# Optimization experiments

Measured on AMD Instinct MI355X. Metric: run time of the kernel, lower is better.

The kernel has to match this reference:

```python
import jax, jax.numpy as jnp
import numpy as np

INPUT_DIM = 1024
OUTPUT_DIM = 1024
DEGREE = 8


def setup_inputs() -> dict:
    key = jax.random.key(0)
    k1, k2 = jax.random.split(key)
    x = jax.random.normal(k1, (8192, INPUT_DIM), dtype=jnp.float32)
    std = 1.0 / (INPUT_DIM * (DEGREE + 1))
    cheby_coeffs = jax.random.normal(k2, (INPUT_DIM, OUTPUT_DIM, DEGREE + 1), dtype=jnp.float32) * std
    return {"x": x, "cheby_coeffs": cheby_coeffs}


def reference(x, cheby_coeffs):
    # x: [B, I]; cheby_coeffs: [I, O, D+1]
    degree = cheby_coeffs.shape[-1] - 1
    t = jnp.clip(jnp.tanh(x), -0.999, 0.999)            # [B, I]
    theta = jnp.arccos(t)[..., None]                     # [B, I, 1]
    arange = jnp.arange(degree + 1, dtype=x.dtype)       # [D+1]
    basis = jnp.cos(theta * arange)                      # [B, I, D+1] Chebyshev T_d(t)
    y = jnp.einsum('bid,iod->bo', basis, cheby_coeffs)   # [B, O]
    return y
```

## Files before the change

kernel.cpp:

```cpp
#include <hip/hip_runtime.h>
#include <stdint.h>

#define B_ROWS 8192
#define I_DIM  1024
#define N_DIM  1024
#define NDEG   9
#define K_DIM  (I_DIM * (NDEG-1))

#define BM 256
#define BN 128
#define BK 64
#define NT (K_DIM / BK)

typedef __attribute__((ext_vector_type(8)))  short short8;
typedef __attribute__((ext_vector_type(16))) float f32x16;

__device__ __forceinline__ unsigned short f2bf(float f) {
  union { float f; uint32_t u; } v; v.f = f;
  uint32_t u = v.u;
  u += 0x7FFFu + ((u >> 16) & 1u);
  return (unsigned short)(u >> 16);
}

__device__ __forceinline__ float bf2f(unsigned short h) {
  union { uint32_t u; float f; } v; v.u = ((uint32_t)h) << 16;
  return v.f;
}

__device__ __forceinline__ int h2(int r) { return (r >> 2) & 7; }

__global__ __launch_bounds__(256) void prep_kernel(const float* __restrict__ x,
                                                   const float* __restrict__ cf,
                                                   unsigned short* __restrict__ A,
                                                   unsigned short* __restrict__ Bt,
                                                   float* __restrict__ bias,
                                                   int repack_blocks) {
  __shared__ unsigned short L[32][584];
  const int tid = threadIdx.x;

  if ((int)blockIdx.x < repack_blocks) {
    const int bx = blockIdx.x;
    const int i0 = (bx & 31) * 32;
    const int o0 = (bx >> 5) * 64;

    #pragma unroll
    for (int j = 0; j < 18; ++j) {
      const int f4  = j * 256 + tid;
      const int il  = f4 / 144;
      const int odq = f4 % 144;
      const float4 v = *reinterpret_cast<const float4*>(
          cf + ((size_t)(i0 + il) * N_DIM + o0) * NDEG + (size_t)odq * 4);
      ushort4 w;
      w.x = f2bf(v.x); w.y = f2bf(v.y); w.z = f2bf(v.z); w.w = f2bf(v.w);
      *reinterpret_cast<ushort4*>(&L[il][odq * 4]) = w;
    }
    __syncthreads();

    for (int od = tid; od < 576; od += 256) {
      const int o = od / 9, d = od % 9;
      if (d == 0) {
        float s = 0.f;
        #pragma unroll
        for (int il = 0; il < 32; ++il) s += bf2f(L[il][od]);
        atomicAdd(&bias[o0 + o], s);
      } else {
        const size_t base = (size_t)(o0 + o) * K_DIM + (size_t)(d - 1) * I_DIM + i0;
        #pragma unroll
        for (int ci = 0; ci < 4; ++ci) {
          uint32_t uu[4];
          #pragma unroll
          for (int p = 0; p < 4; ++p) {
            unsigned short lo = L[ci * 8 + p * 2 + 0][od];
            unsigned short hi = L[ci * 8 + p * 2 + 1][od];
            uu[p] = (uint32_t)lo | ((uint32_t)hi << 16);
          }
          uint4 u; u.x = uu[0]; u.y = uu[1]; u.z = uu[2]; u.w = uu[3];
          *reinterpret_cast<uint4*>(Bt + base + ci * 8) = u;
        }
      }
    }
  } else {
    const int b  = blockIdx.x - repack_blocks;
    const int i0 = tid * 4;
    const float4 xv = *reinterpret_cast<const float4*>(x + (size_t)b * I_DIM + i0);
    float t[4];
    t[0] = fminf(fmaxf(tanhf(xv.x), -0.999f), 0.999f);
    t[1] = fminf(fmaxf(tanhf(xv.y), -0.999f), 0.999f);
    t[2] = fminf(fmaxf(tanhf(xv.z), -0.999f), 0.999f);
    t[3] = fminf(fmaxf(tanhf(xv.w), -0.999f), 0.999f);

    unsigned short* outb = A + (size_t)b * K_DIM + i0;
    float Tp[4] = {1.f, 1.f, 1.f, 1.f};
    float Tc[4] = {t[0], t[1], t[2], t[3]};
    #pragma unroll
    for (int d = 1; d < NDEG; ++d) {
      ushort4 o4;
      o4.x = f2bf(Tc[0]); o4.y = f2bf(Tc[1]); o4.z = f2bf(Tc[2]); o4.w = f2bf(Tc[3]);
      *reinterpret_cast<ushort4*>(outb + (size_t)(d - 1) * I_DIM) = o4;
      if (d < NDEG - 1) {
        #pragma unroll
        for (int j = 0; j < 4; ++j) {
          float Tn = 2.0f * t[j] * Tc[j] - Tp[j];
          Tp[j] = Tc[j]; Tc[j] = Tn;
        }
      }
    }
  }
}

__global__ __launch_bounds__(512, 2) void gemm_kernel(const unsigned short* __restrict__ A,
                                                      const unsigned short* __restrict__ Bt,
                                                      const float* __restrict__ bias,
                                                      float* __restrict__ C) {
  extern __shared__ unsigned short sm[];
  const int tid  = threadIdx.x;
  const int lane = tid & 63;
  const int wave = tid >> 6;
  const int l31  = lane & 31;
  const int half = lane >> 5;
  const int wm   = wave >> 1;
  const int wn   = wave & 1;
  const int m0   = blockIdx.x * BM;
  const int n0   = blockIdx.y * BN;

  const int sr   = tid >> 3;
  const int slot = tid & 7;

  const unsigned short* Abase = A  + (size_t)m0 * K_DIM;
  const unsigned short* Bbase = Bt + (size_t)n0 * K_DIM;

  f32x16 acc[2][2];
  #pragma unroll
  for (int a = 0; a < 2; ++a)
    #pragma unroll
    for (int b = 0; b < 2; ++b)
      #pragma unroll
      for (int r = 0; r < 16; ++r)
        acc[a][b][r] = 0.f;

#define STAGE_A(s, bf, kk) { const int r_ = (s)*64 + sr; const int gc_ = slot ^ h2(r_);     \
    __builtin_amdgcn_global_load_lds(                                                       \
        (const __attribute__((address_space(1))) void*)(Abase + (size_t)r_*K_DIM + (kk) + gc_*8), \
        (__attribute__((address_space(3))) void*)&sm[(bf)*16384 + r_*64 + slot*8], 16, 0, 0); }
#define STAGE_B(s, bf, kk) { const int r_ = (s)*64 + sr; const int gc_ = slot ^ h2(r_);     \
    __builtin_amdgcn_global_load_lds(                                                       \
        (const __attribute__((address_space(1))) void*)(Bbase + (size_t)r_*K_DIM + (kk) + gc_*8), \
        (__attribute__((address_space(3))) void*)&sm[49152 + (bf)*8192 + r_*64 + slot*8], 16, 0, 0); }
#define STAGE6(bf, kk) { STAGE_A(0, bf, kk) STAGE_A(1, bf, kk) STAGE_A(2, bf, kk) STAGE_A(3, bf, kk) \
                         STAGE_B(0, bf, kk) STAGE_B(1, bf, kk) }

  STAGE6(0, 0)
  STAGE6(1, BK)
  asm volatile("s_waitcnt vmcnt(6)" ::: "memory");
  __builtin_amdgcn_s_barrier();

  const int rowA0 = wm * 64 + l31;
  const int rowA1 = wm * 64 + 32 + l31;
  const int rowB0 = wn * 64 + l31;
  const int rowB1 = wn * 64 + 32 + l31;

  int cur = 0;
  for (int kt = 0; kt < NT; ++kt) {
    const unsigned short* Asc = &sm[cur * 16384];
    const unsigned short* Bsc = &sm[49152 + cur * 8192];
    const int s2 = (cur == 0) ? 2 : cur - 1;

    short8 av[2][4], bv[2][4];
    #pragma unroll
    for (int ks = 0; ks < 4; ++ks) {
      const int c = ks * 2 + half;
      av[0][ks] = *reinterpret_cast<const short8*>(&Asc[rowA0 * 64 + (c ^ h2(rowA0)) * 8]);
      av[1][ks] = *reinterpret_cast<const short8*>(&Asc[rowA1 * 64 + (c ^ h2(rowA1)) * 8]);
      bv[0][ks] = *reinterpret_cast<const short8*>(&Bsc[rowB0 * 64 + (c ^ h2(rowB0)) * 8]);
      bv[1][ks] = *reinterpret_cast<const short8*>(&Bsc[rowB1 * 64 + (c ^ h2(rowB1)) * 8]);
    }

    if (kt + 2 < NT) { STAGE6(s2, (kt + 2) * BK) }

    __builtin_amdgcn_s_setprio(1);
    #pragma unroll
    for (int ks = 0; ks < 4; ++ks) {
      acc[0][0] = __builtin_amdgcn_mfma_f32_32x32x16_bf16(av[0][ks], bv[0][ks], acc[0][0], 0, 0, 0);
      acc[0][1] = __builtin_amdgcn_mfma_f32_32x32x16_bf16(av[0][ks], bv[1][ks], acc[0][1], 0, 0, 0);
      acc[1][0] = __builtin_amdgcn_mfma_f32_32x32x16_bf16(av[1][ks], bv[0][ks], acc[1][0], 0, 0, 0);
      acc[1][1] = __builtin_amdgcn_mfma_f32_32x32x16_bf16(av[1][ks], bv[1][ks], acc[1][1], 0, 0, 0);
    }
    __builtin_amdgcn_s_setprio(0);

    if (kt < NT - 1) {
      if (kt < NT - 2) asm volatile("s_waitcnt vmcnt(6)" ::: "memory");
      else             asm volatile("s_waitcnt vmcnt(0)" ::: "memory");
      __builtin_amdgcn_s_barrier();
    }
    cur = (cur == 2) ? 0 : cur + 1;
  }
#undef STAGE_A
#undef STAGE_B
#undef STAGE6

  #pragma unroll
  for (int ni = 0; ni < 2; ++ni) {
    const int col  = n0 + wn * 64 + ni * 32 + l31;
    const float bc = bias[col];
    #pragma unroll
    for (int mi = 0; mi < 2; ++mi) {
      const int rbase = m0 + wm * 64 + mi * 32 + 4 * half;
      #pragma unroll
      for (int r = 0; r < 16; ++r) {
        const int row = rbase + (r & 3) + 8 * (r >> 2);
        C[(size_t)row * N_DIM + col] = acc[mi][ni][r] + bc;
      }
    }
  }
}

extern "C" void kernel_launch(void* const* d_in, const int* in_sizes, int n_in,
                              void* d_out, int out_size, void* d_ws, size_t ws_size,
                              hipStream_t stream) {
  const float* x      = (const float*)d_in[0];
  const float* coeffs = (const float*)d_in[1];
  float* y            = (float*)d_out;

  const size_t bt_bytes = (size_t)N_DIM * K_DIM * sizeof(unsigned short);
  unsigned short* Bt = (unsigned short*)d_ws;
  float* bias        = (float*)((char*)d_ws + bt_bytes);
  unsigned short* A  = (unsigned short*)((char*)d_ws + bt_bytes + 4096);

  hipMemsetAsync(bias, 0, N_DIM * sizeof(float), stream);

  hipFuncSetAttribute((const void*)gemm_kernel,
                      hipFuncAttributeMaxDynamicSharedMemorySize, 147456);

  size_t avail    = (ws_size > bt_bytes + 4096) ? (ws_size - bt_bytes - 4096) : 0;
  size_t rows_fit = avail / ((size_t)K_DIM * sizeof(unsigned short));
  int m_chunk = (int)((rows_fit / BM) * BM);
  if (m_chunk > B_ROWS) m_chunk = B_ROWS;
  if (m_chunk < BM)     m_chunk = BM;

  for (int m0 = 0; m0 < B_ROWS; m0 += m_chunk) {
    int mc = B_ROWS - m0; if (mc > m_chunk) mc = m_chunk;
    const int rb = (m0 == 0) ? 512 : 0;
    prep_kernel<<<rb + mc, 256, 0, stream>>>(x + (size_t)m0 * I_DIM, coeffs, A, Bt, bias, rb);
    gemm_kernel<<<dim3(mc / BM, N_DIM / BN), 512, 147456, stream>>>(
        A, Bt, bias, y + (size_t)m0 * N_DIM);
  }
}
```

Before: 286.6 us.

## Store shared-memory tiles in MFMA fragment order and use fast tanh

Changes the shared-memory staging layout so each wave's global_load_lds writes 32-row by 16-column fragments laid out in the exact per-lane order the MFMA reads use. Each lane then reads a contiguous 16-byte slot, which removes the XOR swizzle and per-lane row address arithmetic. The global loads now fetch 16-element chunks from 32 rows per instruction, which may change global coalescing. The prep kernel also swaps tanhf for an exp-based fast tanh, cutting transcendental cost with slightly lower accuracy.

```diff
diff --git a/kernel.cpp b/kernel.cpp
--- a/kernel.cpp
+++ b/kernel.cpp
@@ -27,7 +27,10 @@
   return v.f;
 }
 
-__device__ __forceinline__ int h2(int r) { return (r >> 2) & 7; }
+__device__ __forceinline__ float fast_tanh(float x) {
+  float e = __expf(2.0f * x);
+  return 1.0f - __fdividef(2.0f, e + 1.0f);
+}
 
 __global__ __launch_bounds__(256) void prep_kernel(const float* __restrict__ x,
                                                    const float* __restrict__ cf,
@@ -84,10 +87,10 @@
     const int i0 = tid * 4;
     const float4 xv = *reinterpret_cast<const float4*>(x + (size_t)b * I_DIM + i0);
     float t[4];
-    t[0] = fminf(fmaxf(tanhf(xv.x), -0.999f), 0.999f);
-    t[1] = fminf(fmaxf(tanhf(xv.y), -0.999f), 0.999f);
-    t[2] = fminf(fmaxf(tanhf(xv.z), -0.999f), 0.999f);
-    t[3] = fminf(fmaxf(tanhf(xv.w), -0.999f), 0.999f);
+    t[0] = fminf(fmaxf(fast_tanh(xv.x), -0.999f), 0.999f);
+    t[1] = fminf(fmaxf(fast_tanh(xv.y), -0.999f), 0.999f);
+    t[2] = fminf(fmaxf(fast_tanh(xv.z), -0.999f), 0.999f);
+    t[3] = fminf(fmaxf(fast_tanh(xv.w), -0.999f), 0.999f);
 
     unsigned short* outb = A + (size_t)b * K_DIM + i0;
     float Tp[4] = {1.f, 1.f, 1.f, 1.f};
@@ -123,11 +126,9 @@
   const int m0   = blockIdx.x * BM;
   const int n0   = blockIdx.y * BN;
 
-  const int sr   = tid >> 3;
-  const int slot = tid & 7;
-
   const unsigned short* Abase = A  + (size_t)m0 * K_DIM;
   const unsigned short* Bbase = Bt + (size_t)n0 * K_DIM;
+  const size_t rowoff = (size_t)l31 * K_DIM + half * 8;
 
   f32x16 acc[2][2];
   #pragma unroll
@@ -138,41 +139,38 @@
       for (int r = 0; r < 16; ++r)
         acc[a][b][r] = 0.f;
 
-#define STAGE_A(s, bf, kk) { const int r_ = (s)*64 + sr; const int gc_ = slot ^ h2(r_);     \
+#define STAGE_A(pa, bf, kk) {                                                               \
+    const int g_ = (pa) >> 2, c2_ = (pa) & 3;                                               \
     __builtin_amdgcn_global_load_lds(                                                       \
-        (const __attribute__((address_space(1))) void*)(Abase + (size_t)r_*K_DIM + (kk) + gc_*8), \
-        (__attribute__((address_space(3))) void*)&sm[(bf)*16384 + r_*64 + slot*8], 16, 0, 0); }
-#define STAGE_B(s, bf, kk) { const int r_ = (s)*64 + sr; const int gc_ = slot ^ h2(r_);     \
+        (const __attribute__((address_space(1))) void*)(Abase + (size_t)(g_*32)*K_DIM + rowoff + (kk) + c2_*16), \
+        (__attribute__((address_space(3))) void*)&sm[(bf)*16384 + (pa)*512 + lane*8], 16, 0, 0); }
+#define STAGE_B(pb, bf, kk) {                                                               \
+    const int g_ = (pb) >> 2, c2_ = (pb) & 3;                                               \
     __builtin_amdgcn_global_load_lds(                                                       \
-        (const __attribute__((address_space(1))) void*)(Bbase + (size_t)r_*K_DIM + (kk) + gc_*8), \
-        (__attribute__((address_space(3))) void*)&sm[49152 + (bf)*8192 + r_*64 + slot*8], 16, 0, 0); }
-#define STAGE6(bf, kk) { STAGE_A(0, bf, kk) STAGE_A(1, bf, kk) STAGE_A(2, bf, kk) STAGE_A(3, bf, kk) \
-                         STAGE_B(0, bf, kk) STAGE_B(1, bf, kk) }
+        (const __attribute__((address_space(1))) void*)(Bbase + (size_t)(g_*32)*K_DIM + rowoff + (kk) + c2_*16), \
+        (__attribute__((address_space(3))) void*)&sm[49152 + (bf)*8192 + (pb)*512 + lane*8], 16, 0, 0); }
+#define STAGE6(bf, kk) { STAGE_A(wave*4 + 0, bf, kk) STAGE_A(wave*4 + 1, bf, kk)            \
+                         STAGE_A(wave*4 + 2, bf, kk) STAGE_A(wave*4 + 3, bf, kk)            \
+                         STAGE_B(wave*2 + 0, bf, kk) STAGE_B(wave*2 + 1, bf, kk) }
 
   STAGE6(0, 0)
   STAGE6(1, BK)
   asm volatile("s_waitcnt vmcnt(6)" ::: "memory");
   __builtin_amdgcn_s_barrier();
 
-  const int rowA0 = wm * 64 + l31;
-  const int rowA1 = wm * 64 + 32 + l31;
-  const int rowB0 = wn * 64 + l31;
-  const int rowB1 = wn * 64 + 32 + l31;
-
   int cur = 0;
   for (int kt = 0; kt < NT; ++kt) {
-    const unsigned short* Asc = &sm[cur * 16384];
-    const unsigned short* Bsc = &sm[49152 + cur * 8192];
+    const unsigned short* Asc = &sm[cur * 16384 + lane * 8];
+    const unsigned short* Bsc = &sm[49152 + cur * 8192 + lane * 8];
     const int s2 = (cur == 0) ? 2 : cur - 1;
 
     short8 av[2][4], bv[2][4];
     #pragma unroll
     for (int ks = 0; ks < 4; ++ks) {
-      const int c = ks * 2 + half;
-      av[0][ks] = *reinterpret_cast<const short8*>(&Asc[rowA0 * 64 + (c ^ h2(rowA0)) * 8]);
-      av[1][ks] = *reinterpret_cast<const short8*>(&Asc[rowA1 * 64 + (c ^ h2(rowA1)) * 8]);
-      bv[0][ks] = *reinterpret_cast<const short8*>(&Bsc[rowB0 * 64 + (c ^ h2(rowB0)) * 8]);
-      bv[1][ks] = *reinterpret_cast<const short8*>(&Bsc[rowB1 * 64 + (c ^ h2(rowB1)) * 8]);
+      av[0][ks] = *reinterpret_cast<const short8*>(&Asc[((wm*2 + 0)*4 + ks) * 512]);
+      av[1][ks] = *reinterpret_cast<const short8*>(&Asc[((wm*2 + 1)*4 + ks) * 512]);
+      bv[0][ks] = *reinterpret_cast<const short8*>(&Bsc[((wn*2 + 0)*4 + ks) * 512]);
+      bv[1][ks] = *reinterpret_cast<const short8*>(&Bsc[((wn*2 + 1)*4 + ks) * 512]);
     }
 
     if (kt + 2 < NT) { STAGE6(s2, (kt + 2) * BK) }
```

After: 314.2 us. 1.1x slower.
